# Kernel tuning notes

Hardware: AMD Instinct MI355X
Metric: run time of the kernel (lower is better)

## Reference

```python
import jax, jax.numpy as jnp
import numpy as np
import math

DIM = 512
HEADS = 8
DHEAD = DIM // HEADS            # 64
NB_FEATURES = int(DHEAD * math.log(DHEAD))  # 266
B, N = 2, 2048
CHUNK = 128                     # chunk size for the causal scan
EPS = 1e-4


def gaussian_orthogonal_random_matrix(nb_rows, nb_cols, rng):
    # blocks of orthogonal rows (Q^T of QR of a gaussian), scaled by chi-distributed norms
    blocks = []
    n_full = nb_rows // nb_cols
    for _ in range(n_full):
        q, _ = np.linalg.qr(rng.standard_normal((nb_cols, nb_cols)))
        blocks.append(q.T)
    rem = nb_rows - n_full * nb_cols
    if rem > 0:
        q, _ = np.linalg.qr(rng.standard_normal((nb_cols, nb_cols)))
        blocks.append(q.T[:rem])
    mat = np.concatenate(blocks, axis=0)
    multiplier = np.linalg.norm(rng.standard_normal((nb_rows, nb_cols)), axis=1)
    return (multiplier[:, None] * mat).astype(np.float32)


def setup_inputs() -> dict:
    key = jax.random.key(0)
    k1, k2, k3 = jax.random.split(key, 3)
    rng = np.random.default_rng(0)
    x = jax.random.normal(k1, (B, N, DIM), dtype=jnp.float32)
    w_qkv = jax.random.normal(k2, (DIM, 3 * DIM), dtype=jnp.float32) / math.sqrt(DIM)
    w_out = jax.random.normal(k3, (DIM, DIM), dtype=jnp.float32) / math.sqrt(DIM)
    b_out = jnp.zeros((DIM,), dtype=jnp.float32)
    proj = jnp.asarray(gaussian_orthogonal_random_matrix(NB_FEATURES, DHEAD, rng))
    return {"x": x, "w_qkv": w_qkv, "w_out": w_out, "b_out": b_out, "proj": proj}


def softmax_kernel(data, proj, is_query):
    # data: [b,h,n,d], proj: [m,d]
    d = data.shape[-1]
    data_normalizer = d ** -0.25
    ratio = proj.shape[0] ** -0.5
    data_dash = jnp.einsum('bhnd,md->bhnm', data_normalizer * data, proj)
    diag_data = jnp.sum(data * data, axis=-1, keepdims=True) * 0.5 * (data_normalizer ** 2)
    if is_query:
        stab = jnp.max(data_dash, axis=-1, keepdims=True)
    else:
        stab = jnp.max(data_dash)
    return ratio * (jnp.exp(data_dash - diag_data - stab) + EPS)


def causal_linear_attention(q, k, v, chunk=CHUNK):
    # q,k: [b,h,n,m]; v: [b,h,n,d]
    # out_n = sum_m q_nm * (sum_{i<=n} k_im v_i) / (sum_{i<=n} k_im)   (per-feature normalization,
    # identical to causal_linear_attention_noncuda), computed in chunks for memory efficiency.
    b, h, n, m = q.shape
    d = v.shape[-1]
    nc = n // chunk
    qc = jnp.moveaxis(q.reshape(b, h, nc, chunk, m), 2, 0)  # [nc,b,h,C,m]
    kc = jnp.moveaxis(k.reshape(b, h, nc, chunk, m), 2, 0)
    vc = jnp.moveaxis(v.reshape(b, h, nc, chunk, d), 2, 0)

    def step(carry, inp):
        kv_state, ksum_state = carry            # [b,h,m,d], [b,h,m]
        qch, kch, vch = inp                     # [b,h,C,m], [b,h,C,m], [b,h,C,d]
        ksum = ksum_state[:, :, None, :] + jnp.cumsum(kch, axis=2)          # [b,h,C,m]
        ctx = kv_state[:, :, None, :, :] + jnp.cumsum(
            jnp.einsum('bhcm,bhcd->bhcmd', kch, vch), axis=2)               # [b,h,C,m,d]
        out = jnp.einsum('bhcm,bhcmd->bhcd', qch, ctx / ksum[..., None])
        return (ctx[:, :, -1], ksum[:, :, -1]), out

    init = (jnp.zeros((b, h, m, d), q.dtype), jnp.zeros((b, h, m), q.dtype))
    _, outs = jax.lax.scan(step, init, (qc, kc, vc))
    return jnp.moveaxis(outs, 0, 2).reshape(b, h, n, d)


def reference(x, w_qkv, w_out, b_out, proj):
    b, n, _ = x.shape
    qkv = x @ w_qkv                                   # [b,n,3*dim]
    q, k, v = jnp.split(qkv, 3, axis=-1)
    split = lambda t: t.reshape(b, n, HEADS, DHEAD).transpose(0, 2, 1, 3)  # b h n d
    q, k, v = split(q), split(k), split(v)
    qp = softmax_kernel(q, proj, is_query=True)       # [b,h,n,m]
    kp = softmax_kernel(k, proj, is_query=False)
    out = causal_linear_attention(qp, kp, v)          # [b,h,n,d]
    out = out.transpose(0, 2, 1, 3).reshape(b, n, DIM)
    return out @ w_out + b_out
```

## Files before the change

### kernel.cpp

```cpp
#include <hip/hip_runtime.h>
#include <math.h>

#define DIMX 512
#define NHEADS 8
#define DH 64
#define MF 266
#define MP 272
#define MPS 288
#define NB 2
#define NSEQ 2048
#define NROWS (NB*NSEQ)
#define NBH 16
#define CHK 64
#define NCH 32
#define EPSF 1e-4f
#define LDT 40
#define LDP 72

typedef __attribute__((ext_vector_type(8))) short short8;
typedef __attribute__((ext_vector_type(4))) float f32x4;
typedef unsigned short ushort_t;

__device__ __forceinline__ unsigned fkey(float f){
    unsigned u = __float_as_uint(f);
    return (f < 0.0f) ? ~u : (u | 0x80000000u);
}
__device__ __forceinline__ float fdec(unsigned k){
    unsigned u = (k & 0x80000000u) ? (k & 0x7fffffffu) : ~k;
    return __uint_as_float(u);
}
__device__ __forceinline__ float b2f(ushort_t u){
    return __uint_as_float(((unsigned)u) << 16);
}

__device__ __forceinline__ void bsplit(float a, ushort_t& h, ushort_t& l){
    unsigned u = __float_as_uint(a);
    unsigned r = (u + 0x7fffu + ((u >> 16) & 1u)) & 0xffff0000u;
    h = (ushort_t)(r >> 16);
    float res = a - __uint_as_float(r);
    unsigned v = __float_as_uint(res);
    unsigned r2 = v + 0x7fffu + ((v >> 16) & 1u);
    l = (ushort_t)(r2 >> 16);
}

__global__ __launch_bounds__(256) void split_kernel(
    const float* __restrict__ A, ushort_t* __restrict__ H, ushort_t* __restrict__ L, int total4)
{
    int i = blockIdx.x * 256 + threadIdx.x;
    if (i >= total4) return;
    float4 f = ((const float4*)A)[i];
    ushort_t h0,h1,h2,h3,l0,l1,l2,l3;
    bsplit(f.x,h0,l0); bsplit(f.y,h1,l1); bsplit(f.z,h2,l2); bsplit(f.w,h3,l3);
    ((ushort4*)H)[i] = make_ushort4(h0,h1,h2,h3);
    ((ushort4*)L)[i] = make_ushort4(l0,l1,l2,l3);
}

__global__ __launch_bounds__(256) void splitT_kernel(
    const float* __restrict__ W, ushort_t* __restrict__ Th, ushort_t* __restrict__ Tl,
    int K, int N)
{
    __shared__ ushort_t Sh[64][72], Sl[64][72];
    const int k0 = blockIdx.y * 64, n0 = blockIdx.x * 64;
    const int tid = threadIdx.x;
    {
        const int kk = tid >> 4, nq = (tid & 15) * 4;
        for (int p = 0; p < 4; p++) {
            int k = p*16 + kk;
            float4 f = *(const float4*)&W[(size_t)(k0 + k)*N + n0 + nq];
            ushort_t h, l;
            bsplit(f.x,h,l); Sh[nq+0][k]=h; Sl[nq+0][k]=l;
            bsplit(f.y,h,l); Sh[nq+1][k]=h; Sl[nq+1][k]=l;
            bsplit(f.z,h,l); Sh[nq+2][k]=h; Sl[nq+2][k]=l;
            bsplit(f.w,h,l); Sh[nq+3][k]=h; Sl[nq+3][k]=l;
        }
    }
    __syncthreads();
    {
        const int n = tid >> 2, ks = (tid & 3) * 16;
        for (int q = 0; q < 2; q++) {
            uint4 vh = *(const uint4*)&Sh[n][ks + q*8];
            uint4 vl = *(const uint4*)&Sl[n][ks + q*8];
            *(uint4*)&Th[(size_t)(n0 + n)*K + k0 + ks + q*8] = vh;
            *(uint4*)&Tl[(size_t)(n0 + n)*K + k0 + ks + q*8] = vl;
        }
    }
}

__global__ __launch_bounds__(256) void splitP_kernel(
    const float* __restrict__ proj, ushort_t* __restrict__ ph, ushort_t* __restrict__ pl,
    unsigned* __restrict__ gmax, float nrm)
{
    int idx = blockIdx.x * 256 + threadIdx.x;
    if (idx == 0) *gmax = 0u;
    if (idx >= MPS*64/4) return;
    int m = idx >> 4, kq = (idx & 15) * 4;
    ushort4 h4 = make_ushort4(0,0,0,0), l4 = make_ushort4(0,0,0,0);
    if (m < MF) {
        float4 f = *(const float4*)&proj[m*64 + kq];
        ushort_t hh[4], ll[4];
        bsplit(f.x*nrm,hh[0],ll[0]); bsplit(f.y*nrm,hh[1],ll[1]);
        bsplit(f.z*nrm,hh[2],ll[2]); bsplit(f.w*nrm,hh[3],ll[3]);
        h4 = make_ushort4(hh[0],hh[1],hh[2],hh[3]);
        l4 = make_ushort4(ll[0],ll[1],ll[2],ll[3]);
    }
    *(ushort4*)&ph[(size_t)m*64 + kq] = h4;
    *(ushort4*)&pl[(size_t)m*64 + kq] = l4;
}

__global__ __launch_bounds__(256) void gemm_bf16s(
    const ushort_t* __restrict__ Ah, const ushort_t* __restrict__ Al,
    const ushort_t* __restrict__ Bh, const ushort_t* __restrict__ Bl,
    const float* __restrict__ bias, float* __restrict__ C,
    int M, int N, int K)
{
    __shared__ ushort_t sAh[128*LDT], sAl[128*LDT], sBh[128*LDT], sBl[128*LDT];
    const int tid = threadIdx.x;
    const int m0 = blockIdx.y * 128, n0 = blockIdx.x * 128;
    const int lane = tid & 63, w = tid >> 6;
    const int wr = w >> 1, wc = w & 1;
    const int lr = lane & 15;
    const int lsu = (lane >> 4) * 8;
    const int r = tid >> 1, sg = (tid & 1) * 16;
    const size_t gA = (size_t)(m0 + r)*K + sg;
    const size_t gB = (size_t)(n0 + r)*K + sg;

    f32x4 acc[4][4];
    #pragma unroll
    for (int i=0;i<4;i++)
        #pragma unroll
        for (int j=0;j<4;j++) acc[i][j] = (f32x4){0.f,0.f,0.f,0.f};

    for (int k0 = 0; k0 < K; k0 += 32) {
        uint4 a0 = *(const uint4*)&Ah[gA + k0];
        uint4 a1 = *(const uint4*)&Ah[gA + k0 + 8];
        uint4 a2 = *(const uint4*)&Al[gA + k0];
        uint4 a3 = *(const uint4*)&Al[gA + k0 + 8];
        uint4 b0 = *(const uint4*)&Bh[gB + k0];
        uint4 b1 = *(const uint4*)&Bh[gB + k0 + 8];
        uint4 b2 = *(const uint4*)&Bl[gB + k0];
        uint4 b3 = *(const uint4*)&Bl[gB + k0 + 8];
        __syncthreads();
        *(uint4*)&sAh[r*LDT + sg]     = a0;
        *(uint4*)&sAh[r*LDT + sg + 8] = a1;
        *(uint4*)&sAl[r*LDT + sg]     = a2;
        *(uint4*)&sAl[r*LDT + sg + 8] = a3;
        *(uint4*)&sBh[r*LDT + sg]     = b0;
        *(uint4*)&sBh[r*LDT + sg + 8] = b1;
        *(uint4*)&sBl[r*LDT + sg]     = b2;
        *(uint4*)&sBl[r*LDT + sg + 8] = b3;
        __syncthreads();
        short8 afh[4], afl[4], bfh[4], bfl[4];
        #pragma unroll
        for (int f = 0; f < 4; f++) {
            int ra = (wr*64 + f*16 + lr)*LDT + lsu;
            int rb = (wc*64 + f*16 + lr)*LDT + lsu;
            afh[f] = *(const short8*)&sAh[ra];
            afl[f] = *(const short8*)&sAl[ra];
            bfh[f] = *(const short8*)&sBh[rb];
            bfl[f] = *(const short8*)&sBl[rb];
        }
        #pragma unroll
        for (int i = 0; i < 4; i++)
            #pragma unroll
            for (int j = 0; j < 4; j++) {
                acc[i][j] = __builtin_amdgcn_mfma_f32_16x16x32_bf16(afh[i], bfh[j], acc[i][j], 0, 0, 0);
                acc[i][j] = __builtin_amdgcn_mfma_f32_16x16x32_bf16(afh[i], bfl[j], acc[i][j], 0, 0, 0);
                acc[i][j] = __builtin_amdgcn_mfma_f32_16x16x32_bf16(afl[i], bfh[j], acc[i][j], 0, 0, 0);
            }
    }
    const int crow = (lane >> 4) * 4, ccol = lane & 15;
    #pragma unroll
    for (int i = 0; i < 4; i++) {
        #pragma unroll
        for (int j = 0; j < 4; j++) {
            int col = n0 + wc*64 + j*16 + ccol;
            float bb = bias ? bias[col] : 0.f;
            #pragma unroll
            for (int rr = 0; rr < 4; rr++) {
                int row = m0 + wr*64 + i*16 + crow + rr;
                C[(size_t)row*N + col] = acc[i][j][rr] + bb;
            }
        }
    }
}

__global__ __launch_bounds__(256) void feat_mfma4(
    const float* __restrict__ qkv,
    const ushort_t* __restrict__ pjh, const ushort_t* __restrict__ pjl,
    ushort_t* __restrict__ qph, ushort_t* __restrict__ qpl,
    ushort_t* __restrict__ kph, ushort_t* __restrict__ kpl,
    float* __restrict__ diag_out, unsigned* __restrict__ gmax, float ratio)
{
    const int tid = threadIdx.x;
    const bool isq = (blockIdx.z == 0);
    const int coff = isq ? 0 : DIMX;
    ushort_t* __restrict__ oh = isq ? qph : kph;
    ushort_t* __restrict__ ol = isq ? qpl : kpl;
    const int bh = blockIdx.y, b = bh >> 3, h = bh & 7;
    const int n0 = blockIdx.x * 64;
    const int lane = tid & 63, w = tid >> 6;
    const int cn = lane & 15, g = lane >> 4;

    short8 bDh[2], bDl[2];
    float dg;
    {
        const int row = w*16 + cn;
        const float* src = &qkv[(size_t)(b*NSEQ + n0 + row)*(3*DIMX) + coff + h*DH];
        float4 u0 = *(const float4*)&src[g*8];
        float4 u1 = *(const float4*)&src[g*8 + 4];
        float4 u2 = *(const float4*)&src[32 + g*8];
        float4 u3 = *(const float4*)&src[32 + g*8 + 4];
        float v0[8] = {u0.x,u0.y,u0.z,u0.w,u1.x,u1.y,u1.z,u1.w};
        float v1[8] = {u2.x,u2.y,u2.z,u2.w,u3.x,u3.y,u3.z,u3.w};
        float ss = 0.f;
        #pragma unroll
        for (int p = 0; p < 8; p++) ss = fmaf(v0[p],v0[p], fmaf(v1[p],v1[p], ss));
        ss += __shfl_xor(ss, 16, 64);
        ss += __shfl_xor(ss, 32, 64);
        dg = 0.0625f * ss;
        #pragma unroll
        for (int p = 0; p < 8; p++) {
            ushort_t hh2, ll2;
            bsplit(v0[p], hh2, ll2); bDh[0][p] = (short)hh2; bDl[0][p] = (short)ll2;
            bsplit(v1[p], hh2, ll2); bDh[1][p] = (short)hh2; bDl[1][p] = (short)ll2;
        }
    }
    f32x4 acc[18];
    #pragma unroll
    for (int t = 0; t < 18; t++) acc[t] = (f32x4){0.f,0.f,0.f,0.f};
    #pragma unroll
    for (int mt = 0; mt < 18; ++mt) {
        const size_t rb = (size_t)(mt*16 + cn)*64 + g*8;
        short8 a0h = *(const short8*)&pjh[rb];
        short8 a1h = *(const short8*)&pjh[rb + 32];
        short8 a0l = *(const short8*)&pjl[rb];
        short8 a1l = *(const short8*)&pjl[rb + 32];
        acc[mt] = __builtin_amdgcn_mfma_f32_16x16x32_bf16(a0h, bDh[0], acc[mt], 0, 0, 0);
        acc[mt] = __builtin_amdgcn_mfma_f32_16x16x32_bf16(a0h, bDl[0], acc[mt], 0, 0, 0);
        acc[mt] = __builtin_amdgcn_mfma_f32_16x16x32_bf16(a0l, bDh[0], acc[mt], 0, 0, 0);
        acc[mt] = __builtin_amdgcn_mfma_f32_16x16x32_bf16(a1h, bDh[1], acc[mt], 0, 0, 0);
        acc[mt] = __builtin_amdgcn_mfma_f32_16x16x32_bf16(a1h, bDl[1], acc[mt], 0, 0, 0);
        acc[mt] = __builtin_amdgcn_mfma_f32_16x16x32_bf16(a1l, bDh[1], acc[mt], 0, 0, 0);
    }
    const size_t orow = ((size_t)bh*NSEQ + n0 + w*16 + cn)*MPS;
    const int mbase0 = g*4;

    if (isq) {
        float mx = -1e30f;
        #pragma unroll
        for (int mt = 0; mt < 18; ++mt) {
            #pragma unroll
            for (int rr = 0; rr < 4; rr++) {
                int m = mt*16 + mbase0 + rr;
                if (m < MF) mx = fmaxf(mx, acc[mt][rr]);
            }
        }
        mx = fmaxf(mx, __shfl_xor(mx, 16, 64));
        mx = fmaxf(mx, __shfl_xor(mx, 32, 64));
        const float sub = dg + mx;
        #pragma unroll
        for (int mt = 0; mt < 18; ++mt) {
            ushort_t hh[4], ll[4];
            #pragma unroll
            for (int rr = 0; rr < 4; rr++) {
                int m = mt*16 + mbase0 + rr;
                float v = (m < MF) ? ratio*(expf(acc[mt][rr] - sub) + EPSF) : 0.f;
                bsplit(v, hh[rr], ll[rr]);
            }
            *(ushort4*)&oh[orow + mt*16 + mbase0] = make_ushort4(hh[0],hh[1],hh[2],hh[3]);
            *(ushort4*)&ol[orow + mt*16 + mbase0] = make_ushort4(ll[0],ll[1],ll[2],ll[3]);
        }
    } else {
        if (g == 0) diag_out[(size_t)bh*NSEQ + n0 + w*16 + cn] = dg;
        float wm = -1e30f;
        #pragma unroll
        for (int mt = 0; mt < 18; ++mt) {
            ushort_t hh[4], ll[4];
            #pragma unroll
            for (int rr = 0; rr < 4; rr++) {
                int m = mt*16 + mbase0 + rr;
                float v = (m < MF) ? acc[mt][rr] : 0.f;
                if (m < MF) wm = fmaxf(wm, v);
                bsplit(v, hh[rr], ll[rr]);
            }
            *(ushort4*)&oh[orow + mt*16 + mbase0] = make_ushort4(hh[0],hh[1],hh[2],hh[3]);
            *(ushort4*)&ol[orow + mt*16 + mbase0] = make_ushort4(ll[0],ll[1],ll[2],ll[3]);
        }
        #pragma unroll
        for (int o = 1; o < 64; o <<= 1) wm = fmaxf(wm, __shfl_xor(wm, o, 64));
        if (lane == 0) atomicMax(gmax, fkey(wm));
    }
}

__global__ __launch_bounds__(256) void kexp_kernel(
    ushort_t* __restrict__ kph, ushort_t* __restrict__ kpl,
    const float* __restrict__ diagk, const unsigned* __restrict__ gmax, float ratio)
{
    unsigned gid = blockIdx.x * 256u + threadIdx.x;
    if (gid >= (unsigned)(NBH*NSEQ*(MPS/4))) return;
    unsigned row = gid / (MPS/4);
    int mq = (int)(gid % (MPS/4)) * 4;
    const float stab = fdec(*gmax);
    const float dg = diagk[row];
    size_t idx = (size_t)row*MPS + mq;
    ushort4 h4 = *(const ushort4*)&kph[idx];
    ushort4 l4 = *(const ushort4*)&kpl[idx];
    float dv[4] = {b2f(h4.x)+b2f(l4.x), b2f(h4.y)+b2f(l4.y),
                   b2f(h4.z)+b2f(l4.z), b2f(h4.w)+b2f(l4.w)};
    ushort_t hh[4], ll[4];
    #pragma unroll
    for (int j = 0; j < 4; j++) {
        float kv = (mq + j < MF) ? ratio * (expf(dv[j] - dg - stab) + EPSF) : 0.f;
        bsplit(kv, hh[j], ll[j]);
    }
    *(ushort4*)&kph[idx] = make_ushort4(hh[0],hh[1],hh[2],hh[3]);
    *(ushort4*)&kpl[idx] = make_ushort4(ll[0],ll[1],ll[2],ll[3]);
}

__global__ __launch_bounds__(320) void chunk_sums_kernel(
    const ushort_t* __restrict__ kph, const ushort_t* __restrict__ kpl,
    const float* __restrict__ qkv,
    float* __restrict__ ckvT, float* __restrict__ cksum)
{
    __shared__ float vs[CHK][DH];
    const int tid = threadIdx.x;
    const int c = blockIdx.x, bh = blockIdx.y, b = bh >> 3, h = bh & 7;
    for (int idx = tid; idx < CHK*16; idx += 320) {
        int i = idx >> 4, q = idx & 15;
        *(float4*)&vs[i][q*4] =
            *(const float4*)&qkv[(size_t)(b*NSEQ + c*CHK + i)*(3*DIMX) + 2*DIMX + h*DH + q*4];
    }
    __syncthreads();
    if (tid >= 272) return;
    const int mg = tid % 68, dg = tid / 68;
    float acc[4][16] = {};
    float ks[4] = {0.f,0.f,0.f,0.f};
    const size_t kbase = (size_t)(bh*NSEQ + c*CHK)*MPS + mg*4;
    for (int i = 0; i < CHK; i++) {
        ushort4 kh = *(const ushort4*)&kph[kbase + (size_t)i*MPS];
        ushort4 kl = *(const ushort4*)&kpl[kbase + (size_t)i*MPS];
        float kr[4] = {b2f(kh.x)+b2f(kl.x), b2f(kh.y)+b2f(kl.y),
                       b2f(kh.z)+b2f(kl.z), b2f(kh.w)+b2f(kl.w)};
        if (dg == 0) { ks[0]+=kr[0]; ks[1]+=kr[1]; ks[2]+=kr[2]; ks[3]+=kr[3]; }
        #pragma unroll
        for (int t = 0; t < 4; t++) {
            float4 vv = *(const float4*)&vs[i][dg*16 + t*4];
            float vr[4] = {vv.x,vv.y,vv.z,vv.w};
            #pragma unroll
            for (int mi=0;mi<4;mi++){
                acc[mi][t*4+0] = fmaf(kr[mi], vr[0], acc[mi][t*4+0]);
                acc[mi][t*4+1] = fmaf(kr[mi], vr[1], acc[mi][t*4+1]);
                acc[mi][t*4+2] = fmaf(kr[mi], vr[2], acc[mi][t*4+2]);
                acc[mi][t*4+3] = fmaf(kr[mi], vr[3], acc[mi][t*4+3]);
            }
        }
    }
    const size_t tbase = (size_t)(bh*NCH + c)*64;
    #pragma unroll
    for (int dd = 0; dd < 16; dd++) {
        int d = dg*16 + dd;
        *(float4*)&ckvT[(tbase + d)*MP + mg*4] =
            make_float4(acc[0][dd], acc[1][dd], acc[2][dd], acc[3][dd]);
    }
    if (dg == 0) {
        #pragma unroll
        for (int mi=0;mi<4;mi++)
            cksum[(size_t)(bh*NCH + c)*MP + mg*4 + mi] = ks[mi];
    }
}

__global__ __launch_bounds__(256) void prefix_ckvT_kernel(
    const float* __restrict__ ckvT, ushort_t* __restrict__ cth, ushort_t* __restrict__ ctl)
{
    const int bh = blockIdx.y;
    const int dm = blockIdx.x * 256 + threadIdx.x;
    if (dm >= 64*MPS) return;
    const int d = dm / MPS, m = dm % MPS;
    if (m < MP) {
        float run = 0.f;
        #pragma unroll
        for (int c = 0; c < NCH; c++) {
            size_t row = (size_t)(bh*NCH + c)*64 + d;
            ushort_t h, l;
            bsplit(run, h, l);
            cth[row*MPS + m] = h; ctl[row*MPS + m] = l;
            run += ckvT[row*MP + m];
        }
    } else {
        #pragma unroll
        for (int c = 0; c < NCH; c++) {
            size_t row = (size_t)(bh*NCH + c)*64 + d;
            cth[row*MPS + m] = 0; ctl[row*MPS + m] = 0;
        }
    }
}

__global__ __launch_bounds__(320) void prefix_ksum_kernel(float* __restrict__ cksum)
{
    const int bh = blockIdx.x;
    const int m = threadIdx.x;
    if (m >= MP) return;
    float run = 0.f;
    #pragma unroll
    for (int c = 0; c < NCH; c++) {
        size_t idx = (size_t)(bh*NCH + c)*MP + m;
        float v = cksum[idx];
        cksum[idx] = run;
        run += v;
    }
}

__global__ __launch_bounds__(320) void qprime_kernel(
    ushort_t* __restrict__ qph, ushort_t* __restrict__ qpl,
    const ushort_t* __restrict__ kph, const ushort_t* __restrict__ kpl,
    const float* __restrict__ cksum)
{
    const int c = blockIdx.x, bh = blockIdx.y;
    const int m = threadIdx.x;
    if (m >= MPS) return;
    size_t base = (size_t)(bh*NSEQ + c*CHK)*MPS + m;
    if (m < MF) {
        float run = cksum[(size_t)(bh*NCH + c)*MP + m];
        for (int i = 0; i < CHK; i++) {
            size_t idx = base + (size_t)i*MPS;
            run += b2f(kph[idx]) + b2f(kpl[idx]);
            float q = b2f(qph[idx]) + b2f(qpl[idx]);
            q /= run;
            ushort_t h, l;
            bsplit(q, h, l);
            qph[idx] = h; qpl[idx] = l;
        }
    } else {
        for (int i = 0; i < CHK; i++) {
            size_t idx = base + (size_t)i*MPS;
            qph[idx] = 0; qpl[idx] = 0;
        }
    }
}

__global__ __launch_bounds__(256) void attn_mfma(
    const ushort_t* __restrict__ qph, const ushort_t* __restrict__ qpl,
    const ushort_t* __restrict__ kph, const ushort_t* __restrict__ kpl,
    const ushort_t* __restrict__ cth, const ushort_t* __restrict__ ctl,
    const float* __restrict__ qkv,
    ushort_t* __restrict__ aout_h, ushort_t* __restrict__ aout_l)
{
    __shared__ ushort_t tQh[64*LDT], tQl[64*LDT];
    __shared__ ushort_t tKh[64*LDT], tKl[64*LDT];
    __shared__ ushort_t tSh[64*LDT], tSl[64*LDT];
    __shared__ ushort_t VTh[64*LDP], VTl[64*LDP];
    __shared__ ushort_t Ph[64*LDP],  Pl[64*LDP];
    const int tid = threadIdx.x;
    const int c = blockIdx.x, bh = blockIdx.y, b = bh >> 3, hh = bh & 7;
    const size_t rowg = (size_t)bh*NSEQ + c*CHK;
    const size_t rowx = (size_t)b*NSEQ + c*CHK;
    const size_t sbase = (size_t)(bh*NCH + c)*64;

    {
        const int j = tid >> 2, dq = (tid & 3) * 16;
        const float* vsrc = &qkv[(rowx + j)*(3*DIMX) + 2*DIMX + hh*DH + dq];
        #pragma unroll
        for (int p = 0; p < 4; p++) {
            float4 f = *(const float4*)&vsrc[p*4];
            float vr[4] = {f.x,f.y,f.z,f.w};
            #pragma unroll
            for (int wv = 0; wv < 4; wv++) {
                ushort_t h, l;
                bsplit(vr[wv], h, l);
                VTh[(dq + p*4 + wv)*LDP + j] = h;
                VTl[(dq + p*4 + wv)*LDP + j] = l;
            }
        }
    }

    const int lane = tid & 63, w = tid >> 6;
    const int wr = w >> 1, wc = w & 1;
    const int fr = lane & 15, fk = (lane >> 4) * 8;
    const int srow = tid >> 2, sseg = (tid & 3) * 8;
    f32x4 accP[2][2], accO[2][2];
    #pragma unroll
    for (int i=0;i<2;i++)
        #pragma unroll
        for (int j=0;j<2;j++){ accP[i][j]=(f32x4){0,0,0,0}; accO[i][j]=(f32x4){0,0,0,0}; }

    for (int m0 = 0; m0 < MPS; m0 += 32) {
        uint4 gq_h = *(const uint4*)&qph[(rowg + srow)*MPS + m0 + sseg];
        uint4 gq_l = *(const uint4*)&qpl[(rowg + srow)*MPS + m0 + sseg];
        uint4 gk_h = *(const uint4*)&kph[(rowg + srow)*MPS + m0 + sseg];
        uint4 gk_l = *(const uint4*)&kpl[(rowg + srow)*MPS + m0 + sseg];
        uint4 gs_h = *(const uint4*)&cth[(sbase + srow)*MPS + m0 + sseg];
        uint4 gs_l = *(const uint4*)&ctl[(sbase + srow)*MPS + m0 + sseg];
        __syncthreads();
        *(uint4*)&tQh[srow*LDT + sseg] = gq_h;
        *(uint4*)&tQl[srow*LDT + sseg] = gq_l;
        *(uint4*)&tKh[srow*LDT + sseg] = gk_h;
        *(uint4*)&tKl[srow*LDT + sseg] = gk_l;
        *(uint4*)&tSh[srow*LDT + sseg] = gs_h;
        *(uint4*)&tSl[srow*LDT + sseg] = gs_l;
        __syncthreads();
        short8 aQh[2], aQl[2], bKh[2], bKl[2], bSh[2], bSl[2];
        #pragma unroll
        for (int f = 0; f < 2; f++) {
            int ra = (wr*32 + f*16 + fr)*LDT + fk;
            int rb = (wc*32 + f*16 + fr)*LDT + fk;
            aQh[f] = *(const short8*)&tQh[ra];
            aQl[f] = *(const short8*)&tQl[ra];
            bKh[f] = *(const short8*)&tKh[rb];
            bKl[f] = *(const short8*)&tKl[rb];
            bSh[f] = *(const short8*)&tSh[rb];
            bSl[f] = *(const short8*)&tSl[rb];
        }
        #pragma unroll
        for (int i = 0; i < 2; i++)
            #pragma unroll
            for (int j = 0; j < 2; j++) {
                accP[i][j] = __builtin_amdgcn_mfma_f32_16x16x32_bf16(aQh[i], bKh[j], accP[i][j], 0, 0, 0);
                accP[i][j] = __builtin_amdgcn_mfma_f32_16x16x32_bf16(aQh[i], bKl[j], accP[i][j], 0, 0, 0);
                accP[i][j] = __builtin_amdgcn_mfma_f32_16x16x32_bf16(aQl[i], bKh[j], accP[i][j], 0, 0, 0);
                accO[i][j] = __builtin_amdgcn_mfma_f32_16x16x32_bf16(aQh[i], bSh[j], accO[i][j], 0, 0, 0);
                accO[i][j] = __builtin_amdgcn_mfma_f32_16x16x32_bf16(aQh[i], bSl[j], accO[i][j], 0, 0, 0);
                accO[i][j] = __builtin_amdgcn_mfma_f32_16x16x32_bf16(aQl[i], bSh[j], accO[i][j], 0, 0, 0);
            }
    }

    __syncthreads();
    {
        const int crow = (lane >> 4) * 4, ccol = lane & 15;
        #pragma unroll
        for (int i = 0; i < 2; i++)
            #pragma unroll
            for (int j = 0; j < 2; j++) {
                int colg = wc*32 + j*16 + ccol;
                #pragma unroll
                for (int rr = 0; rr < 4; rr++) {
                    int rowg2 = wr*32 + i*16 + crow + rr;
                    float v = (colg <= rowg2) ? accP[i][j][rr] : 0.f;
                    ushort_t h, l;
                    bsplit(v, h, l);
                    Ph[rowg2*LDP + colg] = h;
                    Pl[rowg2*LDP + colg] = l;
                }
            }
    }
    __syncthreads();

    #pragma unroll
    for (int js = 0; js < 2; js++) {
        short8 aPh[2], aPl[2], bVh[2], bVl[2];
        #pragma unroll
        for (int f = 0; f < 2; f++) {
            int ra = (wr*32 + f*16 + fr)*LDP + js*32 + fk;
            int rb = (wc*32 + f*16 + fr)*LDP + js*32 + fk;
            aPh[f] = *(const short8*)&Ph[ra];
            aPl[f] = *(const short8*)&Pl[ra];
            bVh[f] = *(const short8*)&VTh[rb];
            bVl[f] = *(const short8*)&VTl[rb];
        }
        #pragma unroll
        for (int i = 0; i < 2; i++)
            #pragma unroll
            for (int j = 0; j < 2; j++) {
                accO[i][j] = __builtin_amdgcn_mfma_f32_16x16x32_bf16(aPh[i], bVh[j], accO[i][j], 0, 0, 0);
                accO[i][j] = __builtin_amdgcn_mfma_f32_16x16x32_bf16(aPh[i], bVl[j], accO[i][j], 0, 0, 0);
                accO[i][j] = __builtin_amdgcn_mfma_f32_16x16x32_bf16(aPl[i], bVh[j], accO[i][j], 0, 0, 0);
            }
    }

    __syncthreads();
    {
        const int crow = (lane >> 4) * 4, ccol = lane & 15;
        #pragma unroll
        for (int i = 0; i < 2; i++)
            #pragma unroll
            for (int j = 0; j < 2; j++) {
                int d = wc*32 + j*16 + ccol;
                #pragma unroll
                for (int rr = 0; rr < 4; rr++) {
                    int row = wr*32 + i*16 + crow + rr;
                    ushort_t h, l;
                    bsplit(accO[i][j][rr], h, l);
                    Ph[row*LDP + d] = h;
                    Pl[row*LDP + d] = l;
                }
            }
    }
    __syncthreads();
    #pragma unroll
    for (int p = 0; p < 2; p++) {
        int u = tid + p*256;
        int row = u >> 3, c8 = u & 7;
        size_t o = (rowx + row)*DIMX + hh*DH + c8*8;
        *(uint4*)&aout_h[o] = *(const uint4*)&Ph[row*LDP + c8*8];
        *(uint4*)&aout_l[o] = *(const uint4*)&Pl[row*LDP + c8*8];
    }
}

extern "C" void kernel_launch(void* const* d_in, const int* in_sizes, int n_in,
                              void* d_out, int out_size, void* d_ws, size_t ws_size,
                              hipStream_t stream)
{
    (void)in_sizes; (void)n_in; (void)out_size; (void)ws_size;
    const float* x     = (const float*)d_in[0];
    const float* w_qkv = (const float*)d_in[1];
    const float* w_out = (const float*)d_in[2];
    const float* b_out = (const float*)d_in[3];
    const float* proj  = (const float*)d_in[4];
    float* out = (float*)d_out;

    char* ws = (char*)d_ws;
    size_t off = 0;
    auto alloc = [&](size_t bytes) -> char* {
        char* p = ws + off;
        off += (bytes + 255) & ~(size_t)255;
        return p;
    };
    float* qkv       = (float*)alloc((size_t)NROWS*3*DIMX*sizeof(float));
    float* ckvT      = (float*)alloc((size_t)NBH*NCH*64*MP*sizeof(float));
    ushort_t* qph    = (ushort_t*)alloc((size_t)NBH*NSEQ*MPS*sizeof(ushort_t));
    ushort_t* qpl    = (ushort_t*)alloc((size_t)NBH*NSEQ*MPS*sizeof(ushort_t));
    ushort_t* kph    = (ushort_t*)alloc((size_t)NBH*NSEQ*MPS*sizeof(ushort_t));
    ushort_t* kpl    = (ushort_t*)alloc((size_t)NBH*NSEQ*MPS*sizeof(ushort_t));
    ushort_t* cth    = (ushort_t*)alloc((size_t)NBH*NCH*64*MPS*sizeof(ushort_t));
    ushort_t* ctl    = (ushort_t*)alloc((size_t)NBH*NCH*64*MPS*sizeof(ushort_t));
    float* cksum     = (float*)alloc((size_t)NBH*NCH*MP*sizeof(float));
    float* diagk     = (float*)alloc((size_t)NBH*NSEQ*sizeof(float));
    unsigned* gmax   = (unsigned*)alloc(256);
    ushort_t* xs_h   = (ushort_t*)alloc((size_t)NROWS*DIMX*sizeof(ushort_t));
    ushort_t* xs_l   = (ushort_t*)alloc((size_t)NROWS*DIMX*sizeof(ushort_t));
    ushort_t* wqt_h  = (ushort_t*)alloc((size_t)(3*DIMX)*DIMX*sizeof(ushort_t));
    ushort_t* wqt_l  = (ushort_t*)alloc((size_t)(3*DIMX)*DIMX*sizeof(ushort_t));
    ushort_t* wot_h  = (ushort_t*)alloc((size_t)DIMX*DIMX*sizeof(ushort_t));
    ushort_t* wot_l  = (ushort_t*)alloc((size_t)DIMX*DIMX*sizeof(ushort_t));
    ushort_t* pjh    = (ushort_t*)alloc((size_t)MPS*64*sizeof(ushort_t));
    ushort_t* pjl    = (ushort_t*)alloc((size_t)MPS*64*sizeof(ushort_t));
    ushort_t* aout_h = xs_h;
    ushort_t* aout_l = xs_l;

    const float nrm   = (float)pow(64.0, -0.25);
    const float ratio = (float)(1.0 / sqrt(266.0));

    split_kernel<<<dim3((NROWS*DIMX/4 + 255)/256), 256, 0, stream>>>(x, xs_h, xs_l, NROWS*DIMX/4);
    splitT_kernel<<<dim3(3*DIMX/64, DIMX/64), 256, 0, stream>>>(w_qkv, wqt_h, wqt_l, DIMX, 3*DIMX);
    splitT_kernel<<<dim3(DIMX/64, DIMX/64), 256, 0, stream>>>(w_out, wot_h, wot_l, DIMX, DIMX);
    splitP_kernel<<<dim3((MPS*64/4 + 255)/256), 256, 0, stream>>>(proj, pjh, pjl, gmax, nrm);
    gemm_bf16s<<<dim3(3*DIMX/128, NROWS/128), 256, 0, stream>>>(
        xs_h, xs_l, wqt_h, wqt_l, nullptr, qkv, NROWS, 3*DIMX, DIMX);
    feat_mfma4<<<dim3(32, 16, 2), 256, 0, stream>>>(
        qkv, pjh, pjl, qph, qpl, kph, kpl, diagk, gmax, ratio);
    kexp_kernel<<<dim3((NBH*NSEQ*(MPS/4) + 255)/256), 256, 0, stream>>>(
        kph, kpl, diagk, gmax, ratio);
    chunk_sums_kernel<<<dim3(NCH, NBH), 320, 0, stream>>>(kph, kpl, qkv, ckvT, cksum);
    prefix_ckvT_kernel<<<dim3((64*MPS + 255)/256, NBH), 256, 0, stream>>>(ckvT, cth, ctl);
    prefix_ksum_kernel<<<dim3(NBH), 320, 0, stream>>>(cksum);
    qprime_kernel<<<dim3(NCH, NBH), 320, 0, stream>>>(qph, qpl, kph, kpl, cksum);
    attn_mfma<<<dim3(NCH, NBH), 256, 0, stream>>>(
        qph, qpl, kph, kpl, cth, ctl, qkv, aout_h, aout_l);
    gemm_bf16s<<<dim3(DIMX/128, NROWS/128), 256, 0, stream>>>(
        aout_h, aout_l, wot_h, wot_l, b_out, out, NROWS, DIMX, DIMX);
}
```

Baseline: 255.0 us.

## Split feature projection across two blocks per row tile and defer query exp

The feature kernel now launches twice as many blocks, each computing half of the 18 projection tiles, so more waves run concurrently with fewer accumulator registers each. Because a block no longer sees the full feature row, the query row max is combined through per-row atomicMax and the query exponentiation moves into the separate exp pass, which now handles both q and k. The cost is an extra full read-modify-write of the query feature buffers, a memset of the row-max array, and more atomics.

Result: slower. 294.0 us (+15.3%).

```diff
diff --git a/kernel.cpp b/kernel.cpp
--- a/kernel.cpp
+++ b/kernel.cpp
@@ -184,20 +184,23 @@
     }
 }
 
-__global__ __launch_bounds__(256) void feat_mfma4(
+__global__ __launch_bounds__(256) void feat_mfma5(
     const float* __restrict__ qkv,
     const ushort_t* __restrict__ pjh, const ushort_t* __restrict__ pjl,
     ushort_t* __restrict__ qph, ushort_t* __restrict__ qpl,
     ushort_t* __restrict__ kph, ushort_t* __restrict__ kpl,
-    float* __restrict__ diag_out, unsigned* __restrict__ gmax, float ratio)
+    float* __restrict__ diagq, float* __restrict__ diagk,
+    unsigned* __restrict__ rowmax, unsigned* __restrict__ gmax)
 {
     const int tid = threadIdx.x;
     const bool isq = (blockIdx.z == 0);
     const int coff = isq ? 0 : DIMX;
     ushort_t* __restrict__ oh = isq ? qph : kph;
     ushort_t* __restrict__ ol = isq ? qpl : kpl;
+    float* __restrict__ dgo = isq ? diagq : diagk;
     const int bh = blockIdx.y, b = bh >> 3, h = bh & 7;
-    const int n0 = blockIdx.x * 64;
+    const int mhalf = blockIdx.x & 1;
+    const int n0 = (blockIdx.x >> 1) * 64;
     const int lane = tid & 63, w = tid >> 6;
     const int cn = lane & 15, g = lane >> 4;
 
@@ -225,96 +228,82 @@
             bsplit(v1[p], hh2, ll2); bDh[1][p] = (short)hh2; bDl[1][p] = (short)ll2;
         }
     }
-    f32x4 acc[18];
-    #pragma unroll
-    for (int t = 0; t < 18; t++) acc[t] = (f32x4){0.f,0.f,0.f,0.f};
-    #pragma unroll
-    for (int mt = 0; mt < 18; ++mt) {
-        const size_t rb = (size_t)(mt*16 + cn)*64 + g*8;
+    const size_t rowidx = (size_t)bh*NSEQ + n0 + w*16 + cn;
+    if (mhalf == 0 && g == 0) dgo[rowidx] = dg;
+
+    const int mbase = mhalf * 9;
+    f32x4 acc[9];
+    #pragma unroll
+    for (int t = 0; t < 9; t++) acc[t] = (f32x4){0.f,0.f,0.f,0.f};
+    #pragma unroll
+    for (int t = 0; t < 9; ++t) {
+        const size_t rb = (size_t)((mbase + t)*16 + cn)*64 + g*8;
         short8 a0h = *(const short8*)&pjh[rb];
         short8 a1h = *(const short8*)&pjh[rb + 32];
         short8 a0l = *(const short8*)&pjl[rb];
         short8 a1l = *(const short8*)&pjl[rb + 32];
-        acc[mt] = __builtin_amdgcn_mfma_f32_16x16x32_bf16(a0h, bDh[0], acc[mt], 0, 0, 0);
-        acc[mt] = __builtin_amdgcn_mfma_f32_16x16x32_bf16(a0h, bDl[0], acc[mt], 0, 0, 0);
-        acc[mt] = __builtin_amdgcn_mfma_f32_16x16x32_bf16(a0l, bDh[0], acc[mt], 0, 0, 0);
-        acc[mt] = __builtin_amdgcn_mfma_f32_16x16x32_bf16(a1h, bDh[1], acc[mt], 0, 0, 0);
-        acc[mt] = __builtin_amdgcn_mfma_f32_16x16x32_bf16(a1h, bDl[1], acc[mt], 0, 0, 0);
-        acc[mt] = __builtin_amdgcn_mfma_f32_16x16x32_bf16(a1l, bDh[1], acc[mt], 0, 0, 0);
-    }
-    const size_t orow = ((size_t)bh*NSEQ + n0 + w*16 + cn)*MPS;
-    const int mbase0 = g*4;
-
+        acc[t] = __builtin_amdgcn_mfma_f32_16x16x32_bf16(a0h, bDh[0], acc[t], 0, 0, 0);
+        acc[t] = __builtin_amdgcn_mfma_f32_16x16x32_bf16(a0h, bDl[0], acc[t], 0, 0, 0);
+        acc[t] = __builtin_amdgcn_mfma_f32_16x16x32_bf16(a0l, bDh[0], acc[t], 0, 0, 0);
+        acc[t] = __builtin_amdgcn_mfma_f32_16x16x32_bf16(a1h, bDh[1], acc[t], 0, 0, 0);
+        acc[t] = __builtin_amdgcn_mfma_f32_16x16x32_bf16(a1h, bDl[1], acc[t], 0, 0, 0);
+        acc[t] = __builtin_amdgcn_mfma_f32_16x16x32_bf16(a1l, bDh[1], acc[t], 0, 0, 0);
+    }
+    const size_t orow = rowidx * MPS;
+    const int mb0 = g*4;
+    float mx = -1e30f;
+    #pragma unroll
+    for (int t = 0; t < 9; ++t) {
+        ushort_t hh[4], ll[4];
+        #pragma unroll
+        for (int rr = 0; rr < 4; rr++) {
+            int m = (mbase + t)*16 + mb0 + rr;
+            float v = (m < MF) ? acc[t][rr] : 0.f;
+            if (m < MF) mx = fmaxf(mx, v);
+            bsplit(v, hh[rr], ll[rr]);
+        }
+        *(ushort4*)&oh[orow + (mbase + t)*16 + mb0] = make_ushort4(hh[0],hh[1],hh[2],hh[3]);
+        *(ushort4*)&ol[orow + (mbase + t)*16 + mb0] = make_ushort4(ll[0],ll[1],ll[2],ll[3]);
+    }
     if (isq) {
-        float mx = -1e30f;
-        #pragma unroll
-        for (int mt = 0; mt < 18; ++mt) {
-            #pragma unroll
-            for (int rr = 0; rr < 4; rr++) {
-                int m = mt*16 + mbase0 + rr;
-                if (m < MF) mx = fmaxf(mx, acc[mt][rr]);
-            }
-        }
         mx = fmaxf(mx, __shfl_xor(mx, 16, 64));
         mx = fmaxf(mx, __shfl_xor(mx, 32, 64));
-        const float sub = dg + mx;
-        #pragma unroll
-        for (int mt = 0; mt < 18; ++mt) {
-            ushort_t hh[4], ll[4];
-            #pragma unroll
-            for (int rr = 0; rr < 4; rr++) {
-                int m = mt*16 + mbase0 + rr;
-                float v = (m < MF) ? ratio*(expf(acc[mt][rr] - sub) + EPSF) : 0.f;
-                bsplit(v, hh[rr], ll[rr]);
-            }
-            *(ushort4*)&oh[orow + mt*16 + mbase0] = make_ushort4(hh[0],hh[1],hh[2],hh[3]);
-            *(ushort4*)&ol[orow + mt*16 + mbase0] = make_ushort4(ll[0],ll[1],ll[2],ll[3]);
-        }
+        if (g == 0) atomicMax(&rowmax[rowidx], fkey(mx));
     } else {
-        if (g == 0) diag_out[(size_t)bh*NSEQ + n0 + w*16 + cn] = dg;
-        float wm = -1e30f;
-        #pragma unroll
-        for (int mt = 0; mt < 18; ++mt) {
-            ushort_t hh[4], ll[4];
-            #pragma unroll
-            for (int rr = 0; rr < 4; rr++) {
-                int m = mt*16 + mbase0 + rr;
-                float v = (m < MF) ? acc[mt][rr] : 0.f;
-                if (m < MF) wm = fmaxf(wm, v);
-                bsplit(v, hh[rr], ll[rr]);
-            }
-            *(ushort4*)&oh[orow + mt*16 + mbase0] = make_ushort4(hh[0],hh[1],hh[2],hh[3]);
-            *(ushort4*)&ol[orow + mt*16 + mbase0] = make_ushort4(ll[0],ll[1],ll[2],ll[3]);
-        }
-        #pragma unroll
-        for (int o = 1; o < 64; o <<= 1) wm = fmaxf(wm, __shfl_xor(wm, o, 64));
-        if (lane == 0) atomicMax(gmax, fkey(wm));
-    }
-}
-
-__global__ __launch_bounds__(256) void kexp_kernel(
+        #pragma unroll
+        for (int o = 1; o < 64; o <<= 1) mx = fmaxf(mx, __shfl_xor(mx, o, 64));
+        if (lane == 0) atomicMax(gmax, fkey(mx));
+    }
+}
+
+__global__ __launch_bounds__(256) void qkexp_kernel(
+    ushort_t* __restrict__ qph, ushort_t* __restrict__ qpl,
     ushort_t* __restrict__ kph, ushort_t* __restrict__ kpl,
-    const float* __restrict__ diagk, const unsigned* __restrict__ gmax, float ratio)
+    const float* __restrict__ diagq, const float* __restrict__ diagk,
+    const unsigned* __restrict__ rowmax, const unsigned* __restrict__ gmax, float ratio)
 {
     unsigned gid = blockIdx.x * 256u + threadIdx.x;
     if (gid >= (unsigned)(NBH*NSEQ*(MPS/4))) return;
+    const bool isq = (blockIdx.y == 0);
     unsigned row = gid / (MPS/4);
     int mq = (int)(gid % (MPS/4)) * 4;
-    const float stab = fdec(*gmax);
-    const float dg = diagk[row];
+    const float sub = isq ? (diagq[row] + fdec(rowmax[row]))
+                          : (diagk[row] + fdec(*gmax));
+    ushort_t* __restrict__ ph = isq ? qph : kph;
+    ushort_t* __restrict__ pl = isq ? qpl : kpl;
     size_t idx = (size_t)row*MPS + mq;
-    ushort4 h4 = *(const ushort4*)&kph[idx];
-    ushort4 l4 = *(const ushort4*)&kpl[idx];
+    ushort4 h4 = *(const ushort4*)&ph[idx];
+    ushort4 l4 = *(const ushort4*)&pl[idx];
     float dv[4] = {b2f(h4.x)+b2f(l4.x), b2f(h4.y)+b2f(l4.y),
                    b2f(h4.z)+b2f(l4.z), b2f(h4.w)+b2f(l4.w)};
     ushort_t hh[4], ll[4];
     #pragma unroll
     for (int j = 0; j < 4; j++) {
-        float kv = (mq + j < MF) ? ratio * (expf(dv[j] - dg - stab) + EPSF) : 0.f;
+        float kv = (mq + j < MF) ? ratio * (expf(dv[j] - sub) + EPSF) : 0.f;
         bsplit(kv, hh[j], ll[j]);
     }
-    *(ushort4*)&kph[idx] = make_ushort4(hh[0],hh[1],hh[2],hh[3]);
-    *(ushort4*)&kpl[idx] = make_ushort4(ll[0],ll[1],ll[2],ll[3]);
+    *(ushort4*)&ph[idx] = make_ushort4(hh[0],hh[1],hh[2],hh[3]);
+    *(ushort4*)&pl[idx] = make_ushort4(ll[0],ll[1],ll[2],ll[3]);
 }
 
 __global__ __launch_bounds__(320) void chunk_sums_kernel(
@@ -623,7 +612,9 @@
     ushort_t* cth    = (ushort_t*)alloc((size_t)NBH*NCH*64*MPS*sizeof(ushort_t));
     ushort_t* ctl    = (ushort_t*)alloc((size_t)NBH*NCH*64*MPS*sizeof(ushort_t));
     float* cksum     = (float*)alloc((size_t)NBH*NCH*MP*sizeof(float));
+    float* diagq     = (float*)alloc((size_t)NBH*NSEQ*sizeof(float));
     float* diagk     = (float*)alloc((size_t)NBH*NSEQ*sizeof(float));
+    unsigned* rowmax = (unsigned*)alloc((size_t)NBH*NSEQ*sizeof(unsigned));
     unsigned* gmax   = (unsigned*)alloc(256);
     ushort_t* xs_h   = (ushort_t*)alloc((size_t)NROWS*DIMX*sizeof(ushort_t));
     ushort_t* xs_l   = (ushort_t*)alloc((size_t)NROWS*DIMX*sizeof(ushort_t));
@@ -639,16 +630,17 @@
     const float nrm   = (float)pow(64.0, -0.25);
     const float ratio = (float)(1.0 / sqrt(266.0));
 
+    hipMemsetAsync(rowmax, 0, (size_t)NBH*NSEQ*sizeof(unsigned), stream);
     split_kernel<<<dim3((NROWS*DIMX/4 + 255)/256), 256, 0, stream>>>(x, xs_h, xs_l, NROWS*DIMX/4);
     splitT_kernel<<<dim3(3*DIMX/64, DIMX/64), 256, 0, stream>>>(w_qkv, wqt_h, wqt_l, DIMX, 3*DIMX);
     splitT_kernel<<<dim3(DIMX/64, DIMX/64), 256, 0, stream>>>(w_out, wot_h, wot_l, DIMX, DIMX);
     splitP_kernel<<<dim3((MPS*64/4 + 255)/256), 256, 0, stream>>>(proj, pjh, pjl, gmax, nrm);
     gemm_bf16s<<<dim3(3*DIMX/128, NROWS/128), 256, 0, stream>>>(
         xs_h, xs_l, wqt_h, wqt_l, nullptr, qkv, NROWS, 3*DIMX, DIMX);
-    feat_mfma4<<<dim3(32, 16, 2), 256, 0, stream>>>(
-        qkv, pjh, pjl, qph, qpl, kph, kpl, diagk, gmax, ratio);
-    kexp_kernel<<<dim3((NBH*NSEQ*(MPS/4) + 255)/256), 256, 0, stream>>>(
-        kph, kpl, diagk, gmax, ratio);
+    feat_mfma5<<<dim3(64, 16, 2), 256, 0, stream>>>(
+        qkv, pjh, pjl, qph, qpl, kph, kpl, diagq, diagk, rowmax, gmax);
+    qkexp_kernel<<<dim3((NBH*NSEQ*(MPS/4) + 255)/256, 2), 256, 0, stream>>>(
+        qph, qpl, kph, kpl, diagq, diagk, rowmax, gmax, ratio);
     chunk_sums_kernel<<<dim3(NCH, NBH), 320, 0, stream>>>(kph, kpl, qkv, ckvT, cksum);
     prefix_ckvT_kernel<<<dim3((64*MPS + 255)/256, NBH), 256, 0, stream>>>(ckvT, cth, ctl);
     prefix_ksum_kernel<<<dim3(NBH), 320, 0, stream>>>(cksum);
```
